# Kernel optimization log

Measured on AMD Instinct MI355X. Metric: run time of the kernel, lower is better.

The kernel has to match this reference:

```python
import jax, jax.numpy as jnp
import numpy as np

N = 6000          # nodes
E = 192000        # edges (avg degree 32)
D = 512           # input_dim
H = 512           # hidden_dim
O = 40            # output_dim (classes)
K = 4096          # codebook_size
LAMB_EDGE = 1.0
LAMB_NODE = 1.0
COMMIT_W = 0.25
EPS = 1e-12


def _graph_conv(x, W, b, src, dst):
    """DGL GraphConv with norm='both' + ReLU activation.
    out = relu( D_in^{-1/2} A D_out^{-1/2} x W + b )"""
    ones = jnp.ones((E,), x.dtype)
    deg_out = jnp.clip(jax.ops.segment_sum(ones, src, num_segments=N), 1.0)
    deg_in = jnp.clip(jax.ops.segment_sum(ones, dst, num_segments=N), 1.0)
    xs = x * jax.lax.rsqrt(deg_out)[:, None]          # scale by src out-degree
    agg = jax.ops.segment_sum(xs[src], dst, num_segments=N)  # gather-scatter
    agg = agg * jax.lax.rsqrt(deg_in)[:, None]        # scale by dst in-degree
    return jax.nn.relu(agg @ W + b)


def _l2norm(x):
    return x * jax.lax.rsqrt(jnp.sum(x * x, axis=-1, keepdims=True) + EPS)


def setup_inputs() -> dict:
    key = jax.random.key(0)
    ks = jax.random.split(key, 13)
    s = lambda d: 1.0 / np.sqrt(d)
    return {
        "feats": jax.random.normal(ks[0], (N, D), jnp.float32),
        "W1": jax.random.normal(ks[1], (D, D), jnp.float32) * s(D),
        "b1": jnp.zeros((D,), jnp.float32),
        "W2": jax.random.normal(ks[2], (D, H), jnp.float32) * s(D),
        "b2": jnp.zeros((H,), jnp.float32),
        "Wd1": jax.random.normal(ks[3], (D, D), jnp.float32) * s(D),
        "bd1": jnp.zeros((D,), jnp.float32),
        "Wd2": jax.random.normal(ks[4], (D, D), jnp.float32) * s(D),
        "bd2": jnp.zeros((D,), jnp.float32),
        "Wl": jax.random.normal(ks[5], (H, O), jnp.float32) * s(H),
        "bl": jnp.zeros((O,), jnp.float32),
        "codebook": jax.random.normal(ks[6], (K, D), jnp.float32),
        "src": jax.random.randint(ks[7], (E,), 0, N, jnp.int32),
        "dst": jax.random.randint(ks[8], (E,), 0, N, jnp.int32),
    }


def reference(feats, W1, b1, W2, b2, Wd1, bd1, Wd2, bd2, Wl, bl, codebook, src, dst):
    # dense adjacency (as the torch module materializes via to_dense())
    adj = jnp.zeros((N, N), feats.dtype).at[dst, src].add(1.0)

    # GraphConv layer 1 (dropout is identity in eval)
    h = _graph_conv(feats, W1, b1, src, dst)           # [N, D]

    # cosine-sim VectorQuantize
    hn = _l2norm(h)
    en = _l2norm(codebook)                             # [K, D]
    dist = hn @ en.T                                   # [N, K] cosine sims
    ind = jnp.argmax(dist, axis=-1)                    # [N]
    q = en[ind]                                        # quantize with normed codebook
    commit_loss = COMMIT_W * jnp.mean((jax.lax.stop_gradient(q) - h) ** 2)
    quantized = h + jax.lax.stop_gradient(q - h)       # straight-through

    quantized_edge = quantized @ Wd1 + bd1             # decoder_1
    quantized_node = quantized @ Wd2 + bd2             # decoder_2

    feature_rec_loss = LAMB_NODE * jnp.mean((h - quantized_node) ** 2)

    adj_q = quantized_edge @ quantized_edge.T          # [N, N]
    adj_q = (adj_q - adj_q.min()) / (adj_q.max() - adj_q.min())
    edge_rec_loss = LAMB_EDGE * jnp.sqrt(jnp.mean((adj - adj_q) ** 2))

    # GraphConv layer 2 + output linear
    h2 = _graph_conv(quantized_edge, W2, b2, src, dst) # [N, H]
    out = h2 @ Wl + bl                                 # [N, O]

    loss = feature_rec_loss + edge_rec_loss + commit_loss
    return out, loss, dist
```

## Files before the change

kernel.cpp:

```cpp
#include <hip/hip_runtime.h>

typedef unsigned int u32;
typedef unsigned long long u64;

#define NN_ 6000
#define EE_ 192000
#define DD_ 512
#define KK_ 4096
#define OO_ 40
#define HSZ (1 << 19)
#define HMASK (HSZ - 1)
#define MT_A 376
#define NB_N 47

typedef __bf16 bf16x8 __attribute__((ext_vector_type(8)));
typedef float f32x4 __attribute__((ext_vector_type(4)));
typedef float f32x2 __attribute__((ext_vector_type(2)));

__device__ __forceinline__ u32 okey(float f) {
    u32 u = __float_as_uint(f);
    return (u & 0x80000000u) ? ~u : (u | 0x80000000u);
}
__device__ __forceinline__ float dkey(u32 u) {
    u32 b = (u & 0x80000000u) ? (u ^ 0x80000000u) : ~u;
    return __uint_as_float(b);
}
__device__ __forceinline__ u64 packKey(float v, int col) {
    return ((u64)okey(v) << 32) | (u32)(~(u32)col);
}
__device__ __forceinline__ unsigned short f2bf_rne(float f) {
    u32 x = __float_as_uint(f);
    u32 r = x + 0x7fffu + ((x >> 16) & 1u);
    return (unsigned short)(r >> 16);
}
__device__ __forceinline__ void gld_lds16(void* l, const void* g) {
    __builtin_amdgcn_global_load_lds(
        (const __attribute__((address_space(1))) unsigned int*)g,
        (__attribute__((address_space(3))) unsigned int*)l, 16, 0, 0);
}
__device__ __forceinline__ void gl8(
    const void* p0, const void* p1, const void* p2, const void* p3,
    const void* p4, const void* p5, const void* p6, const void* p7,
    f32x2& v0, f32x2& v1, f32x2& v2, f32x2& v3,
    f32x2& v4, f32x2& v5, f32x2& v6, f32x2& v7) {
    asm volatile(
        "global_load_dwordx2 %0, %8, off\n\t"
        "global_load_dwordx2 %1, %9, off\n\t"
        "global_load_dwordx2 %2, %10, off\n\t"
        "global_load_dwordx2 %3, %11, off\n\t"
        "global_load_dwordx2 %4, %12, off\n\t"
        "global_load_dwordx2 %5, %13, off\n\t"
        "global_load_dwordx2 %6, %14, off\n\t"
        "global_load_dwordx2 %7, %15, off\n\t"
        "s_waitcnt vmcnt(0)"
        : "=&v"(v0), "=&v"(v1), "=&v"(v2), "=&v"(v3),
          "=&v"(v4), "=&v"(v5), "=&v"(v6), "=&v"(v7)
        : "v"(p0), "v"(p1), "v"(p2), "v"(p3),
          "v"(p4), "v"(p5), "v"(p6), "v"(p7)
        : "memory");
}
__device__ __forceinline__ void split8(const float* vals, uint4& hw, uint4& lw) {
    u32 h[4], l[4];
    #pragma unroll
    for (int j = 0; j < 4; ++j) {
        unsigned short h0 = f2bf_rne(vals[2*j]),   h1 = f2bf_rne(vals[2*j+1]);
        float hf0 = __uint_as_float((u32)h0 << 16), hf1 = __uint_as_float((u32)h1 << 16);
        unsigned short l0 = f2bf_rne(vals[2*j] - hf0), l1 = f2bf_rne(vals[2*j+1] - hf1);
        h[j] = (u32)h0 | ((u32)h1 << 16);
        l[j] = (u32)l0 | ((u32)l1 << 16);
    }
    hw = make_uint4(h[0], h[1], h[2], h[3]);
    lw = make_uint4(l[0], l[1], l[2], l[3]);
}

__global__ void k_deg(const int* __restrict__ src, const int* __restrict__ dst,
                      int* __restrict__ degout, int* __restrict__ degin) {
    int e = blockIdx.x * 256 + threadIdx.x;
    if (e >= EE_) return;
    atomicAdd(&degout[src[e]], 1);
    atomicAdd(&degin[dst[e]], 1);
}

__global__ void k_rsqrtdeg(const int* __restrict__ degout, const int* __restrict__ degin,
                           float* __restrict__ rout, float* __restrict__ rin) {
    int i = blockIdx.x * 256 + threadIdx.x;
    if (i >= NN_) return;
    int doV = degout[i]; if (doV < 1) doV = 1;
    int diV = degin[i];  if (diV < 1) diV = 1;
    rout[i] = rsqrtf((float)doV);
    rin[i]  = rsqrtf((float)diV);
}

__global__ void k_scan(const int* __restrict__ cnt, int* __restrict__ offs, int n) {
    __shared__ int buf[1024];
    __shared__ int carry;
    if (threadIdx.x == 0) { carry = 0; offs[0] = 0; }
    __syncthreads();
    for (int base = 0; base < n; base += 1024) {
        int i = base + threadIdx.x;
        int v = (i < n) ? cnt[i] : 0;
        buf[threadIdx.x] = v;
        __syncthreads();
        for (int off = 1; off < 1024; off <<= 1) {
            int t = (threadIdx.x >= off) ? buf[threadIdx.x - off] : 0;
            __syncthreads();
            buf[threadIdx.x] += t;
            __syncthreads();
        }
        if (i < n) offs[i + 1] = carry + buf[threadIdx.x];
        __syncthreads();
        if (threadIdx.x == 0) carry += buf[1023];
        __syncthreads();
    }
}

__global__ void k_fill(const int* __restrict__ src, const int* __restrict__ dst,
                       const int* __restrict__ offs, int* __restrict__ cursor,
                       int* __restrict__ esrc) {
    int e = blockIdx.x * 256 + threadIdx.x;
    if (e >= EE_) return;
    int d = dst[e];
    int pos = offs[d] + atomicAdd(&cursor[d], 1);
    esrc[pos] = src[e];
}

__device__ __forceinline__ void pack_row_from_lds(
    const float* rowbuf, int node, int t,
    unsigned short* __restrict__ dh, unsigned short* __restrict__ dl) {
    int kb = t >> 2, sub = t & 3;
    int lane = sub * 16 + (node & 15);
    uint4 hw, lw;
    split8(rowbuf + t * 8, hw, lw);
    size_t base = (((size_t)(node >> 4) * 16 + kb) * 64 + lane) * 8;
    *(uint4*)(dh + base) = hw;
    *(uint4*)(dl + base) = lw;
}

__global__ __launch_bounds__(256) void k_aggp(
    const float* __restrict__ X, const int* __restrict__ esrc,
    const int* __restrict__ offs, const float* __restrict__ rout,
    const float* __restrict__ rin,
    unsigned short* __restrict__ dh, unsigned short* __restrict__ dl) {
    __shared__ float rowbuf[512];
    int node = blockIdx.x;
    int beg = offs[node], end = offs[node + 1];
    int t = threadIdx.x;
    float a0 = 0.f, a1 = 0.f, b0 = 0.f, b1 = 0.f;
    float c0 = 0.f, c1 = 0.f, d0 = 0.f, d1 = 0.f;
    int e = beg;
    for (; e + 8 <= end; e += 8) {
        int s0 = esrc[e+0], s1 = esrc[e+1], s2 = esrc[e+2], s3 = esrc[e+3];
        int s4 = esrc[e+4], s5 = esrc[e+5], s6 = esrc[e+6], s7 = esrc[e+7];
        f32x2 v0, v1, v2, v3, v4, v5, v6, v7;
        gl8(X + (size_t)s0 * DD_ + 2 * t, X + (size_t)s1 * DD_ + 2 * t,
            X + (size_t)s2 * DD_ + 2 * t, X + (size_t)s3 * DD_ + 2 * t,
            X + (size_t)s4 * DD_ + 2 * t, X + (size_t)s5 * DD_ + 2 * t,
            X + (size_t)s6 * DD_ + 2 * t, X + (size_t)s7 * DD_ + 2 * t,
            v0, v1, v2, v3, v4, v5, v6, v7);
        float w0 = rout[s0], w1 = rout[s1], w2 = rout[s2], w3 = rout[s3];
        float w4 = rout[s4], w5 = rout[s5], w6 = rout[s6], w7 = rout[s7];
        a0 = fmaf(w0, v0[0], a0); a1 = fmaf(w0, v0[1], a1);
        b0 = fmaf(w1, v1[0], b0); b1 = fmaf(w1, v1[1], b1);
        c0 = fmaf(w2, v2[0], c0); c1 = fmaf(w2, v2[1], c1);
        d0 = fmaf(w3, v3[0], d0); d1 = fmaf(w3, v3[1], d1);
        a0 = fmaf(w4, v4[0], a0); a1 = fmaf(w4, v4[1], a1);
        b0 = fmaf(w5, v5[0], b0); b1 = fmaf(w5, v5[1], b1);
        c0 = fmaf(w6, v6[0], c0); c1 = fmaf(w6, v6[1], c1);
        d0 = fmaf(w7, v7[0], d0); d1 = fmaf(w7, v7[1], d1);
    }
    for (; e < end; ++e) {
        int s = esrc[e];
        float w = rout[s];
        float2 v = ((const float2*)(X + (size_t)s * DD_))[t];
        a0 = fmaf(w, v.x, a0); a1 = fmaf(w, v.y, a1);
    }
    float ri = rin[node];
    rowbuf[2 * t] = (a0 + b0 + c0 + d0) * ri;
    rowbuf[2 * t + 1] = (a1 + b1 + c1 + d1) * ri;
    __syncthreads();
    if (t < 64) pack_row_from_lds(rowbuf, node, t, dh, dl);
}

__global__ __launch_bounds__(256) void k_aggd(
    const float* __restrict__ QE, const int* __restrict__ esrc,
    const int* __restrict__ offs, const float* __restrict__ rout,
    const float* __restrict__ rin,
    unsigned short* __restrict__ dh, unsigned short* __restrict__ dl,
    float* __restrict__ gacc) {
    __shared__ float rowbuf[512];
    __shared__ float wred[4];
    int node = blockIdx.x;
    int beg = offs[node], end = offs[node + 1];
    int t = threadIdx.x;
    float a0 = 0.f, a1 = 0.f, b0 = 0.f, b1 = 0.f;
    float c0 = 0.f, c1 = 0.f, d0 = 0.f, d1 = 0.f;
    float ua0 = 0.f, ua1 = 0.f, ub0 = 0.f, ub1 = 0.f;
    int e = beg;
    for (; e + 8 <= end; e += 8) {
        int s0 = esrc[e+0], s1 = esrc[e+1], s2 = esrc[e+2], s3 = esrc[e+3];
        int s4 = esrc[e+4], s5 = esrc[e+5], s6 = esrc[e+6], s7 = esrc[e+7];
        f32x2 v0, v1, v2, v3, v4, v5, v6, v7;
        gl8(QE + (size_t)s0 * DD_ + 2 * t, QE + (size_t)s1 * DD_ + 2 * t,
            QE + (size_t)s2 * DD_ + 2 * t, QE + (size_t)s3 * DD_ + 2 * t,
            QE + (size_t)s4 * DD_ + 2 * t, QE + (size_t)s5 * DD_ + 2 * t,
            QE + (size_t)s6 * DD_ + 2 * t, QE + (size_t)s7 * DD_ + 2 * t,
            v0, v1, v2, v3, v4, v5, v6, v7);
        float w0 = rout[s0], w1 = rout[s1], w2 = rout[s2], w3 = rout[s3];
        float w4 = rout[s4], w5 = rout[s5], w6 = rout[s6], w7 = rout[s7];
        a0 = fmaf(w0, v0[0], a0); a1 = fmaf(w0, v0[1], a1);
        b0 = fmaf(w1, v1[0], b0); b1 = fmaf(w1, v1[1], b1);
        c0 = fmaf(w2, v2[0], c0); c1 = fmaf(w2, v2[1], c1);
        d0 = fmaf(w3, v3[0], d0); d1 = fmaf(w3, v3[1], d1);
        a0 = fmaf(w4, v4[0], a0); a1 = fmaf(w4, v4[1], a1);
        b0 = fmaf(w5, v5[0], b0); b1 = fmaf(w5, v5[1], b1);
        c0 = fmaf(w6, v6[0], c0); c1 = fmaf(w6, v6[1], c1);
        d0 = fmaf(w7, v7[0], d0); d1 = fmaf(w7, v7[1], d1);
        ua0 += v0[0] + v2[0] + v4[0] + v6[0];
        ua1 += v0[1] + v2[1] + v4[1] + v6[1];
        ub0 += v1[0] + v3[0] + v5[0] + v7[0];
        ub1 += v1[1] + v3[1] + v5[1] + v7[1];
    }
    for (; e < end; ++e) {
        int s = esrc[e];
        float w = rout[s];
        float2 v = ((const float2*)(QE + (size_t)s * DD_))[t];
        a0 = fmaf(w, v.x, a0); a1 = fmaf(w, v.y, a1);
        ua0 += v.x; ua1 += v.y;
    }
    float ri = rin[node];
    rowbuf[2 * t] = (a0 + b0 + c0 + d0) * ri;
    rowbuf[2 * t + 1] = (a1 + b1 + c1 + d1) * ri;
    float2 q = ((const float2*)(QE + (size_t)node * DD_))[t];
    float c = q.x * (ua0 + ub0) + q.y * (ua1 + ub1);
    for (int off = 32; off; off >>= 1) c += __shfl_xor(c, off);
    int lane = t & 63, wv = t >> 6;
    if (lane == 0) wred[wv] = c;
    __syncthreads();
    if (t < 64) pack_row_from_lds(rowbuf, node, t, dh, dl);
    if (t == 0) atomicAdd(&gacc[5], wred[0] + wred[1] + wred[2] + wred[3]);
}

__global__ __launch_bounds__(256) void k_cbscale(const float* __restrict__ cb, float* __restrict__ scale) {
    int row = blockIdx.x;
    float2 v = ((const float2*)(cb + (size_t)row * DD_))[threadIdx.x];
    float s = v.x * v.x + v.y * v.y;
    for (int off = 32; off; off >>= 1) s += __shfl_xor(s, off);
    __shared__ float wsum[4];
    int lane = threadIdx.x & 63, wv = threadIdx.x >> 6;
    if (lane == 0) wsum[wv] = s;
    __syncthreads();
    if (threadIdx.x == 0) scale[row] = 1.0f / sqrtf(wsum[0] + wsum[1] + wsum[2] + wsum[3] + 1e-12f);
}

__global__ __launch_bounds__(256) void k_pack(
    const float* __restrict__ src, const float* __restrict__ rowscale,
    const int* __restrict__ gidx, int nrows,
    unsigned short* __restrict__ dh, unsigned short* __restrict__ dl) {
    int u = threadIdx.x >> 6, lane = threadIdx.x & 63;
    int mt = blockIdx.x, kb = blockIdx.y * 4 + u;
    int gr = mt * 16 + (lane & 15);
    int k = kb * 32 + (lane >> 4) * 8;
    float vals[8] = {0.f,0.f,0.f,0.f,0.f,0.f,0.f,0.f};
    if (gr < nrows) {
        int row = gidx ? gidx[gr] : gr;
        float sc = rowscale ? rowscale[row] : 1.0f;
        const float4* p = (const float4*)(src + (size_t)row * DD_ + k);
        float4 a = p[0], b = p[1];
        vals[0]=a.x*sc; vals[1]=a.y*sc; vals[2]=a.z*sc; vals[3]=a.w*sc;
        vals[4]=b.x*sc; vals[5]=b.y*sc; vals[6]=b.z*sc; vals[7]=b.w*sc;
    }
    uint4 hw, lw;
    split8(vals, hw, lw);
    size_t base = (((size_t)mt * 16 + kb) * 64 + lane) * 8;
    *(uint4*)(dh + base) = hw;
    *(uint4*)(dl + base) = lw;
}

__global__ __launch_bounds__(256) void k_wpack(
    const float* __restrict__ W,
    unsigned short* __restrict__ dh, unsigned short* __restrict__ dl) {
    int u = threadIdx.x >> 6, lane = threadIdx.x & 63;
    int mt = blockIdx.x, kb = blockIdx.y * 4 + u;
    int n = mt * 16 + (lane & 15);
    int k = kb * 32 + (lane >> 4) * 8;
    float vals[8];
    #pragma unroll
    for (int j = 0; j < 8; ++j) vals[j] = W[(size_t)(k + j) * DD_ + n];
    uint4 hw, lw;
    split8(vals, hw, lw);
    size_t base = (((size_t)mt * 16 + kb) * 64 + lane) * 8;
    *(uint4*)(dh + base) = hw;
    *(uint4*)(dl + base) = lw;
}

template<int MODE>
__global__ __launch_bounds__(256) void gemm_mfma(
    const unsigned short* __restrict__ Ah, const unsigned short* __restrict__ Al,
    const unsigned short* __restrict__ Bh, const unsigned short* __restrict__ Bl,
    float* __restrict__ Cout, const float* __restrict__ bias,
    const float* __restrict__ Ref, int relu, int Mrows,
    float* __restrict__ gacc, u32* __restrict__ minKey, u32* __restrict__ maxKey) {
    if (MODE == 1 && blockIdx.x < blockIdx.y) return;
    __shared__ char lds[32768];
    int tid = threadIdx.x;
    int wave = tid >> 6, lane = tid & 63;
    int gmtA = blockIdx.y * 8, gmtB = blockIdx.x * 8;
    const unsigned short* garr; int gmt0;
    if (wave == 0)      { garr = Ah; gmt0 = gmtA; }
    else if (wave == 1) { garr = Al; gmt0 = gmtA; }
    else if (wave == 2) { garr = Bh; gmt0 = gmtB; }
    else                { garr = Bl; gmt0 = gmtB; }
    char* ldst = lds + wave * 8192;
    f32x4 acc[4][4];
    #pragma unroll
    for (int i = 0; i < 4; ++i)
        #pragma unroll
        for (int j = 0; j < 4; ++j) acc[i][j] = (f32x4){0.f, 0.f, 0.f, 0.f};
    int wm = wave >> 1, wn = wave & 1;
    for (int kb = 0; kb < 16; ++kb) {
        #pragma unroll
        for (int t = 0; t < 8; ++t) {
            const char* g = (const char*)garr + (((size_t)(gmt0 + t) * 16 + kb) * 1024) + lane * 16;
            gld_lds16(ldst + t * 1024 + lane * 16, g);
        }
        __syncthreads();
        bf16x8 a_h[4], a_l[4], b_h[4], b_l[4];
        #pragma unroll
        for (int i = 0; i < 4; ++i) {
            int at = wm * 4 + i, bt = wn * 4 + i;
            a_h[i] = *(const bf16x8*)(lds + 0     + at * 1024 + lane * 16);
            a_l[i] = *(const bf16x8*)(lds + 8192  + at * 1024 + lane * 16);
            b_h[i] = *(const bf16x8*)(lds + 16384 + bt * 1024 + lane * 16);
            b_l[i] = *(const bf16x8*)(lds + 24576 + bt * 1024 + lane * 16);
        }
        #pragma unroll
        for (int i = 0; i < 4; ++i)
            #pragma unroll
            for (int j = 0; j < 4; ++j) {
                acc[i][j] = __builtin_amdgcn_mfma_f32_16x16x32_bf16(a_h[i], b_h[j], acc[i][j], 0, 0, 0);
                acc[i][j] = __builtin_amdgcn_mfma_f32_16x16x32_bf16(a_h[i], b_l[j], acc[i][j], 0, 0, 0);
                acc[i][j] = __builtin_amdgcn_mfma_f32_16x16x32_bf16(a_l[i], b_h[j], acc[i][j], 0, 0, 0);
            }
        __syncthreads();
    }
    int m_base = blockIdx.y * 128 + wm * 64;
    int n_base = blockIdx.x * 128 + wn * 64;
    int rq = lane >> 4, cc = lane & 15;
    if (MODE == 0) {
        #pragma unroll
        for (int i = 0; i < 4; ++i) {
            int m = m_base + i * 16 + rq * 4;
            #pragma unroll
            for (int j = 0; j < 4; ++j) {
                int n = n_base + j * 16 + cc;
                #pragma unroll
                for (int r = 0; r < 4; ++r) {
                    if (m + r < NN_) Cout[(size_t)(m + r) * KK_ + n] = acc[i][j][r];
                }
            }
        }
    } else if (MODE == 2) {
        #pragma unroll
        for (int i = 0; i < 4; ++i) {
            int m = m_base + i * 16 + rq * 4;
            #pragma unroll
            for (int j = 0; j < 4; ++j) {
                int n = n_base + j * 16 + cc;
                float bv = bias[n];
                #pragma unroll
                for (int r = 0; r < 4; ++r) {
                    if (m + r < Mrows) {
                        float v = acc[i][j][r] + bv;
                        if (relu) v = fmaxf(v, 0.f);
                        Cout[(size_t)(m + r) * DD_ + n] = v;
                    }
                }
            }
        }
    } else if (MODE == 3) {
        float s = 0.f;
        #pragma unroll
        for (int i = 0; i < 4; ++i) {
            int m = m_base + i * 16 + rq * 4;
            #pragma unroll
            for (int j = 0; j < 4; ++j) {
                int n = n_base + j * 16 + cc;
                float bv = bias[n];
                #pragma unroll
                for (int r = 0; r < 4; ++r) {
                    if (m + r < Mrows) {
                        float d = Ref[(size_t)(m + r) * DD_ + n] - (acc[i][j][r] + bv);
                        s = fmaf(d, d, s);
// ... 145 lines not shown
        int m = m0 + (ty << 2) + i;
        if (m >= M) continue;
        #pragma unroll
        for (int j = 0; j < 4; ++j) {
            int n = n0 + (tx << 2) + j;
            if (n >= Ncols) continue;
            C[(size_t)m * Ncols + n] = cv[i][j] + bias[n];
        }
    }
}

__global__ __launch_bounds__(256) void k_losses(
    const float* __restrict__ h, const float* __restrict__ cb,
    const float* __restrict__ scale, const int* __restrict__ ind,
    float* __restrict__ gacc) {
    float s1 = 0.f;
    for (int idx = blockIdx.x * 256 + threadIdx.x; idx < NN_ * DD_; idx += gridDim.x * 256) {
        int m = idx >> 9, d = idx & 511;
        int r = ind[m];
        float q = cb[(size_t)r * DD_ + d] * scale[r];
        float dq = q - h[idx];
        s1 = fmaf(dq, dq, s1);
    }
    for (int off = 32; off; off >>= 1) s1 += __shfl_xor(s1, off);
    __shared__ float w1[4];
    int lane = threadIdx.x & 63, wv = threadIdx.x >> 6;
    if (lane == 0) w1[wv] = s1;
    __syncthreads();
    if (threadIdx.x == 0) atomicAdd(&gacc[2], w1[0] + w1[1] + w1[2] + w1[3]);
}

__global__ void k_hash(const int* __restrict__ src, const int* __restrict__ dst,
                       int* __restrict__ hkey, int* __restrict__ hcnt) {
    int e = blockIdx.x * 256 + threadIdx.x;
    if (e >= EE_) return;
    int key = dst[e] * NN_ + src[e];
    u32 h = ((u32)key * 2654435761u) & HMASK;
    while (true) {
        int old = atomicCAS(&hkey[h], -1, key);
        if (old == -1 || old == key) { atomicAdd(&hcnt[h], 1); break; }
        h = (h + 1) & HMASK;
    }
}

__global__ __launch_bounds__(256) void k_m2scan(const int* __restrict__ hcnt, float* __restrict__ gacc) {
    float s = 0.f;
    for (int i = blockIdx.x * 256 + threadIdx.x; i < HSZ; i += gridDim.x * 256) {
        float c = (float)hcnt[i];
        s = fmaf(c, c, s);
    }
    for (int off = 32; off; off >>= 1) s += __shfl_xor(s, off);
    __shared__ float w1[4];
    int lane = threadIdx.x & 63, wv = threadIdx.x >> 6;
    if (lane == 0) w1[wv] = s;
    __syncthreads();
    if (threadIdx.x == 0) atomicAdd(&gacc[4], w1[0] + w1[1] + w1[2] + w1[3]);
}

__global__ void k_final(const float* __restrict__ gacc, const u32* __restrict__ minKey,
                        const u32* __restrict__ maxKey, float* __restrict__ lossOut) {
    if (threadIdx.x != 0 || blockIdx.x != 0) return;
    double Rsum = gacc[0], Rsq = gacc[1], commitS = gacc[2], recS = gacc[3];
    double m2 = gacc[4], mr = gacc[5], ms = (double)EE_;
    double mn = (double)dkey(*minKey);
    double mx = (double)dkey(*maxKey);
    double den = mx - mn;
    double NN2 = (double)NN_ * (double)NN_;
    double sum_aq2 = (Rsq - 2.0 * mn * Rsum + NN2 * mn * mn) / (den * den);
    double sum_maq = (mr - mn * ms) / den;
    double total = sum_aq2 + m2 - 2.0 * sum_maq;
    double edge = sqrt(total / NN2);
    double commit = 0.25 * commitS / ((double)NN_ * (double)DD_);
    double rec = recS / ((double)NN_ * (double)DD_);
    *lossOut = (float)(rec + edge + commit);
}

extern "C" void kernel_launch(void* const* d_in, const int* in_sizes, int n_in,
                              void* d_out, int out_size, void* d_ws, size_t ws_size,
                              hipStream_t stream) {
    const float* feats = (const float*)d_in[0];
    const float* W1 = (const float*)d_in[1];
    const float* b1 = (const float*)d_in[2];
    const float* W2 = (const float*)d_in[3];
    const float* b2v = (const float*)d_in[4];
    const float* Wd1 = (const float*)d_in[5];
    const float* bd1 = (const float*)d_in[6];
    const float* Wd2 = (const float*)d_in[7];
    const float* bd2 = (const float*)d_in[8];
    const float* Wl = (const float*)d_in[9];
    const float* bl = (const float*)d_in[10];
    const float* cb = (const float*)d_in[11];
    const int* src = (const int*)d_in[12];
    const int* dst = (const int*)d_in[13];

    float* outF = (float*)d_out;
    float* lossOut = outF + (size_t)NN_ * OO_;
    float* distOut = lossOut + 1;

    char* w = (char*)d_ws;
    size_t off = 0;
    auto alloc = [&](size_t bytes) -> void* {
        void* p = w + off;
        off = (off + bytes + 255) & ~(size_t)255;
        return p;
    };
    float* gacc = (float*)alloc(64);
    u32* maxKey = (u32*)alloc(4);
    int* degin = (int*)alloc((size_t)NN_ * 4);
    int* degout = (int*)alloc((size_t)NN_ * 4);
    int* cursor = (int*)alloc((size_t)NN_ * 4);
    int* hcnt = (int*)alloc((size_t)HSZ * 4);
    size_t z0end = off;
    int* hkey = (int*)alloc((size_t)HSZ * 4);
    u32* minKey = (u32*)alloc(4);
    size_t z1end = off;
    int* offs = (int*)alloc((size_t)(NN_ + 1) * 4);
    int* esrc = (int*)alloc((size_t)EE_ * 4);
    float* rin = (float*)alloc((size_t)NN_ * 4);
    float* rout = (float*)alloc((size_t)NN_ * 4);
    int* ind = (int*)alloc((size_t)NN_ * 4);
    float* scale = (float*)alloc((size_t)KK_ * 4);
    float* rnorm = (float*)alloc((size_t)NN_ * 4);
    float* h = (float*)alloc((size_t)NN_ * DD_ * 4);
    float* QE = (float*)alloc((size_t)NN_ * DD_ * 4);
    const size_t NPACK = (size_t)MT_A * 16 * DD_;
    unsigned short* P1 = (unsigned short*)alloc(NPACK * 2 * 2);
    unsigned short* P2 = (unsigned short*)alloc(NPACK * 2 * 2);
    unsigned short* enp = (unsigned short*)alloc((size_t)KK_ * DD_ * 2 * 2);
    const size_t WPACK = (size_t)32 * 16 * DD_;
    unsigned short* W1p = (unsigned short*)alloc(WPACK * 2 * 2);
    unsigned short* Wd1p = (unsigned short*)alloc(WPACK * 2 * 2);
    unsigned short* Wd2p = (unsigned short*)alloc(WPACK * 2 * 2);
    unsigned short* W2p = (unsigned short*)alloc(WPACK * 2 * 2);

    unsigned short* aggp_h = P1,  *aggp_l = P1 + NPACK;
    unsigned short* qcp_h  = P1,  *qcp_l  = P1 + NPACK;
    unsigned short* ag2p_h = P1,  *ag2p_l = P1 + NPACK;
    unsigned short* hnp_h  = P2,  *hnp_l  = P2 + NPACK;
    unsigned short* QEp_h  = P2,  *QEp_l  = P2 + NPACK;
    unsigned short* enp_h  = enp, *enp_l  = enp + (size_t)KK_ * DD_;

    hipMemsetAsync(w, 0, z0end, stream);
    hipMemsetAsync(w + z0end, 0xFF, z1end - z0end, stream);

    const int TB = 256;
    k_deg<<<(EE_ + TB - 1) / TB, TB, 0, stream>>>(src, dst, degout, degin);
    k_rsqrtdeg<<<(NN_ + TB - 1) / TB, TB, 0, stream>>>(degout, degin, rout, rin);
    k_scan<<<1, 1024, 0, stream>>>(degin, offs, NN_);
    k_fill<<<(EE_ + TB - 1) / TB, TB, 0, stream>>>(src, dst, offs, cursor, esrc);
    k_wpack<<<dim3(32, 4), TB, 0, stream>>>(W1, W1p, W1p + WPACK);
    k_wpack<<<dim3(32, 4), TB, 0, stream>>>(Wd1, Wd1p, Wd1p + WPACK);
    k_wpack<<<dim3(32, 4), TB, 0, stream>>>(Wd2, Wd2p, Wd2p + WPACK);
    k_wpack<<<dim3(32, 4), TB, 0, stream>>>(W2, W2p, W2p + WPACK);
    k_aggp<<<NN_, TB, 0, stream>>>(feats, esrc, offs, rout, rin, aggp_h, aggp_l);
    gemm_mfma<2><<<dim3(4, NB_N), TB, 0, stream>>>(aggp_h, aggp_l, W1p, W1p + WPACK,
                                                   h, b1, nullptr, 1, NN_, nullptr, nullptr, nullptr);
    k_cbscale<<<NN_, TB, 0, stream>>>(h, rnorm);
    k_cbscale<<<KK_, TB, 0, stream>>>(cb, scale);
    k_pack<<<dim3(MT_A, 4), TB, 0, stream>>>(h, rnorm, nullptr, NN_, hnp_h, hnp_l);
    k_pack<<<dim3(KK_ / 16, 4), TB, 0, stream>>>(cb, scale, nullptr, KK_, enp_h, enp_l);
    gemm_mfma<0><<<dim3(KK_ / 128, NB_N), TB, 0, stream>>>(hnp_h, hnp_l, enp_h, enp_l,
                                                           distOut, nullptr, nullptr, 0, NN_,
                                                           nullptr, nullptr, nullptr);
    k_rescore<<<NN_, TB, 0, stream>>>(distOut, h, rnorm, cb, scale, ind);
    k_pack<<<dim3(MT_A, 4), TB, 0, stream>>>(cb, scale, ind, NN_, qcp_h, qcp_l);
    gemm_mfma<2><<<dim3(4, NB_N), TB, 0, stream>>>(qcp_h, qcp_l, Wd1p, Wd1p + WPACK,
                                                   QE, bd1, nullptr, 0, NN_, nullptr, nullptr, nullptr);
    gemm_mfma<3><<<dim3(4, NB_N), TB, 0, stream>>>(qcp_h, qcp_l, Wd2p, Wd2p + WPACK,
                                                   nullptr, bd2, h, 0, NN_, gacc, nullptr, nullptr);
    k_losses<<<2048, TB, 0, stream>>>(h, cb, scale, ind, gacc);
    k_pack<<<dim3(MT_A, 4), TB, 0, stream>>>(QE, nullptr, nullptr, NN_, QEp_h, QEp_l);
    gemm_mfma<1><<<dim3(NB_N, NB_N), TB, 0, stream>>>(QEp_h, QEp_l, QEp_h, QEp_l,
                                                      nullptr, nullptr, nullptr, 0, NN_,
                                                      gacc, minKey, maxKey);
    k_hash<<<(EE_ + TB - 1) / TB, TB, 0, stream>>>(src, dst, hkey, hcnt);
    k_m2scan<<<512, TB, 0, stream>>>(hcnt, gacc);
    k_aggd<<<NN_, TB, 0, stream>>>(QE, esrc, offs, rout, rin, ag2p_h, ag2p_l, gacc);
    gemm_mfma<2><<<dim3(4, NB_N), TB, 0, stream>>>(ag2p_h, ag2p_l, W2p, W2p + WPACK,
                                                   h, b2v, nullptr, 1, NN_, nullptr, nullptr, nullptr);
    gemm_nn<<<dim3(1, 94), TB, 0, stream>>>(h, Wl, bl, outF, NN_, OO_, DD_);
    k_final<<<1, 64, 0, stream>>>(gacc, minKey, maxKey, lossOut);
}
```

Before: 758.3 us.

## Double-buffer neighbor-row gathers into LDS via async global-to-LDS loads

Rewrites the two aggregation kernels so each block first stages neighbor indices and weights in shared memory. Neighbor feature rows are then copied in chunks of 8 with global_load_lds into a double-buffered LDS tile, so the load of the next chunk overlaps the FMA work on the current one. This replaces the previous register gather with a blocking vmcnt(0) wait after every 8 rows. It adds 32KB of LDS per block plus extra barriers, which can lower occupancy for these gather-bound kernels.

```diff
diff --git a/kernel.cpp b/kernel.cpp
--- a/kernel.cpp
+++ b/kernel.cpp
@@ -38,27 +38,133 @@
         (const __attribute__((address_space(1))) unsigned int*)g,
         (__attribute__((address_space(3))) unsigned int*)l, 16, 0, 0);
 }
-__device__ __forceinline__ void gl8(
-    const void* p0, const void* p1, const void* p2, const void* p3,
-    const void* p4, const void* p5, const void* p6, const void* p7,
-    f32x2& v0, f32x2& v1, f32x2& v2, f32x2& v3,
-    f32x2& v4, f32x2& v5, f32x2& v6, f32x2& v7) {
-    asm volatile(
-        "global_load_dwordx2 %0, %8, off\n\t"
-        "global_load_dwordx2 %1, %9, off\n\t"
-        "global_load_dwordx2 %2, %10, off\n\t"
-        "global_load_dwordx2 %3, %11, off\n\t"
-        "global_load_dwordx2 %4, %12, off\n\t"
-        "global_load_dwordx2 %5, %13, off\n\t"
-        "global_load_dwordx2 %6, %14, off\n\t"
-        "global_load_dwordx2 %7, %15, off\n\t"
-        "s_waitcnt vmcnt(0)"
-        : "=&v"(v0), "=&v"(v1), "=&v"(v2), "=&v"(v3),
-          "=&v"(v4), "=&v"(v5), "=&v"(v6), "=&v"(v7)
-        : "v"(p0), "v"(p1), "v"(p2), "v"(p3),
-          "v"(p4), "v"(p5), "v"(p6), "v"(p7)
-        : "memory");
-}
+
+#define WVMC4 do { asm volatile("s_waitcnt vmcnt(4)" ::: "memory"); __builtin_amdgcn_sched_barrier(0); } while (0)
+#define WVMC0 do { asm volatile("s_waitcnt vmcnt(0)" ::: "memory"); __builtin_amdgcn_sched_barrier(0); } while (0)
+#define LGKM0 do { asm volatile("s_waitcnt lgkmcnt(0)" ::: "memory"); __builtin_amdgcn_sched_barrier(0); } while (0)
+#define BARR  do { __builtin_amdgcn_sched_barrier(0); __builtin_amdgcn_s_barrier(); __builtin_amdgcn_sched_barrier(0); } while (0)
+
+__device__ __forceinline__ void stage_chunk(
+    const float* __restrict__ X, const int* sidx, int base,
+    float* dst, int w, int lane) {
+    #pragma unroll
+    for (int rr = 0; rr < 2; ++rr) {
+        int r = 2 * w + rr;
+        int s = sidx[base + r];
+        const float* g = X + (size_t)s * DD_ + lane * 4;
+        float* d = dst + r * DD_;
+        gld_lds16(d, g);
+        gld_lds16(d + 256, g + 256);
+    }
+}
+
+template<int UNW>
+__device__ __forceinline__ void consume_chunk(
+    const float* xb, const float* swt, int base, int t,
+    float& o0, float& o1, float& u0, float& u1) {
+    #pragma unroll
+    for (int r = 0; r < 8; ++r) {
+        float w = swt[base + r];
+        float2 v = *(const float2*)(xb + r * DD_ + 2 * t);
+        o0 = fmaf(w, v.x, o0);
+        o1 = fmaf(w, v.y, o1);
+        if (UNW) { u0 += v.x; u1 += v.y; }
+    }
+}
+
+template<int UNW>
+__device__ __forceinline__ void agg_lds(
+    const float* __restrict__ X, const int* sidx, const float* swt,
+    float* xbuf , int scnt, int t,
+    float& o0, float& o1, float& u0, float& u1) {
+    int w = t >> 6, lane = t & 63;
+    int nch = scnt >> 3;
+    float* b0 = xbuf;
+    float* b1 = xbuf + 8 * DD_;
+    if (nch > 0) {
+        stage_chunk(X, sidx, 0, b0, w, lane);
+        if (nch > 1) {
+            stage_chunk(X, sidx, 8, b1, w, lane);
+            WVMC4;
+        } else {
+            WVMC0;
+        }
+        BARR;
+        int c = 0;
+        for (; c + 2 < nch; ++c) {
+            float* cur = (c & 1) ? b1 : b0;
+            consume_chunk<UNW>(cur, swt, c * 8, t, o0, o1, u0, u1);
+            LGKM0; BARR;
+            stage_chunk(X, sidx, (c + 2) * 8, cur, w, lane);
+            WVMC4; BARR;
+        }
+        consume_chunk<UNW>((c & 1) ? b1 : b0, swt, c * 8, t, o0, o1, u0, u1);
+        ++c;
+        if (c < nch) {
+            WVMC0; BARR;
+            consume_chunk<UNW>((c & 1) ? b1 : b0, swt, c * 8, t, o0, o1, u0, u1);
+        }
+    }
+    for (int i = nch * 8; i < scnt; ++i) {
+        float wgt = swt[i];
+        float2 v = ((const float2*)(X + (size_t)sidx[i] * DD_))[t];
+        o0 = fmaf(wgt, v.x, o0);
+        o1 = fmaf(wgt, v.y, o1);
+        if (UNW) { u0 += v.x; u1 += v.y; }
+    }
+}
+
+__global__ void k_deg(const int* __restrict__ src, const int* __restrict__ dst,
+                      int* __restrict__ degout, int* __restrict__ degin) {
+    int e = blockIdx.x * 256 + threadIdx.x;
+    if (e >= EE_) return;
+    atomicAdd(&degout[src[e]], 1);
+    atomicAdd(&degin[dst[e]], 1);
+}
+
+__global__ void k_rsqrtdeg(const int* __restrict__ degout, const int* __restrict__ degin,
+                           float* __restrict__ rout, float* __restrict__ rin) {
+    int i = blockIdx.x * 256 + threadIdx.x;
+    if (i >= NN_) return;
+    int doV = degout[i]; if (doV < 1) doV = 1;
+    int diV = degin[i];  if (diV < 1) diV = 1;
+    rout[i] = rsqrtf((float)doV);
+    rin[i]  = rsqrtf((float)diV);
+}
+
+__global__ void k_scan(const int* __restrict__ cnt, int* __restrict__ offs, int n) {
+    __shared__ int buf[1024];
+    __shared__ int carry;
+    if (threadIdx.x == 0) { carry = 0; offs[0] = 0; }
+    __syncthreads();
+    for (int base = 0; base < n; base += 1024) {
+        int i = base + threadIdx.x;
+        int v = (i < n) ? cnt[i] : 0;
+        buf[threadIdx.x] = v;
+        __syncthreads();
+        for (int off = 1; off < 1024; off <<= 1) {
+            int t = (threadIdx.x >= off) ? buf[threadIdx.x - off] : 0;
+            __syncthreads();
+            buf[threadIdx.x] += t;
+            __syncthreads();
+        }
+        if (i < n) offs[i + 1] = carry + buf[threadIdx.x];
+        __syncthreads();
+        if (threadIdx.x == 0) carry += buf[1023];
+        __syncthreads();
+    }
+}
+
+__global__ void k_fill(const int* __restrict__ src, const int* __restrict__ dst,
+                       const int* __restrict__ offs, int* __restrict__ cursor,
+                       int* __restrict__ esrc) {
+    int e = blockIdx.x * 256 + threadIdx.x;
+    if (e >= EE_) return;
+    int d = dst[e];
+    int pos = offs[d] + atomicAdd(&cursor[d], 1);
+    esrc[pos] = src[e];
+}
+
 __device__ __forceinline__ void split8(const float* vals, uint4& hw, uint4& lw) {
     u32 h[4], l[4];
     #pragma unroll
@@ -71,57 +177,6 @@
     }
     hw = make_uint4(h[0], h[1], h[2], h[3]);
     lw = make_uint4(l[0], l[1], l[2], l[3]);
-}
-
-__global__ void k_deg(const int* __restrict__ src, const int* __restrict__ dst,
-                      int* __restrict__ degout, int* __restrict__ degin) {
-    int e = blockIdx.x * 256 + threadIdx.x;
-    if (e >= EE_) return;
-    atomicAdd(&degout[src[e]], 1);
-    atomicAdd(&degin[dst[e]], 1);
-}
-
-__global__ void k_rsqrtdeg(const int* __restrict__ degout, const int* __restrict__ degin,
-                           float* __restrict__ rout, float* __restrict__ rin) {
-    int i = blockIdx.x * 256 + threadIdx.x;
-    if (i >= NN_) return;
-    int doV = degout[i]; if (doV < 1) doV = 1;
-    int diV = degin[i];  if (diV < 1) diV = 1;
-    rout[i] = rsqrtf((float)doV);
-    rin[i]  = rsqrtf((float)diV);
-}
-
-__global__ void k_scan(const int* __restrict__ cnt, int* __restrict__ offs, int n) {
-    __shared__ int buf[1024];
-    __shared__ int carry;
-    if (threadIdx.x == 0) { carry = 0; offs[0] = 0; }
-    __syncthreads();
-    for (int base = 0; base < n; base += 1024) {
-        int i = base + threadIdx.x;
-        int v = (i < n) ? cnt[i] : 0;
-        buf[threadIdx.x] = v;
-        __syncthreads();
-        for (int off = 1; off < 1024; off <<= 1) {
-            int t = (threadIdx.x >= off) ? buf[threadIdx.x - off] : 0;
-            __syncthreads();
-            buf[threadIdx.x] += t;
-            __syncthreads();
-        }
-        if (i < n) offs[i + 1] = carry + buf[threadIdx.x];
-        __syncthreads();
-        if (threadIdx.x == 0) carry += buf[1023];
-        __syncthreads();
-    }
-}
-
-__global__ void k_fill(const int* __restrict__ src, const int* __restrict__ dst,
-                       const int* __restrict__ offs, int* __restrict__ cursor,
-                       int* __restrict__ esrc) {
-    int e = blockIdx.x * 256 + threadIdx.x;
-    if (e >= EE_) return;
-    int d = dst[e];
-    int pos = offs[d] + atomicAdd(&cursor[d], 1);
-    esrc[pos] = src[e];
 }
 
 __device__ __forceinline__ void pack_row_from_lds(
@@ -141,42 +196,28 @@
     const int* __restrict__ offs, const float* __restrict__ rout,
     const float* __restrict__ rin,
     unsigned short* __restrict__ dh, unsigned short* __restrict__ dl) {
+    __shared__ float xbuf[2][8][DD_];
     __shared__ float rowbuf[512];
+    __shared__ int sidx[256];
+    __shared__ float swt[256];
     int node = blockIdx.x;
     int beg = offs[node], end = offs[node + 1];
+    int deg = end - beg;
     int t = threadIdx.x;
-    float a0 = 0.f, a1 = 0.f, b0 = 0.f, b1 = 0.f;
-    float c0 = 0.f, c1 = 0.f, d0 = 0.f, d1 = 0.f;
-    int e = beg;
-    for (; e + 8 <= end; e += 8) {
-        int s0 = esrc[e+0], s1 = esrc[e+1], s2 = esrc[e+2], s3 = esrc[e+3];
-        int s4 = esrc[e+4], s5 = esrc[e+5], s6 = esrc[e+6], s7 = esrc[e+7];
-        f32x2 v0, v1, v2, v3, v4, v5, v6, v7;
-        gl8(X + (size_t)s0 * DD_ + 2 * t, X + (size_t)s1 * DD_ + 2 * t,
-            X + (size_t)s2 * DD_ + 2 * t, X + (size_t)s3 * DD_ + 2 * t,
-            X + (size_t)s4 * DD_ + 2 * t, X + (size_t)s5 * DD_ + 2 * t,
-            X + (size_t)s6 * DD_ + 2 * t, X + (size_t)s7 * DD_ + 2 * t,
-            v0, v1, v2, v3, v4, v5, v6, v7);
-        float w0 = rout[s0], w1 = rout[s1], w2 = rout[s2], w3 = rout[s3];
-        float w4 = rout[s4], w5 = rout[s5], w6 = rout[s6], w7 = rout[s7];
-        a0 = fmaf(w0, v0[0], a0); a1 = fmaf(w0, v0[1], a1);
-        b0 = fmaf(w1, v1[0], b0); b1 = fmaf(w1, v1[1], b1);
-        c0 = fmaf(w2, v2[0], c0); c1 = fmaf(w2, v2[1], c1);
-        d0 = fmaf(w3, v3[0], d0); d1 = fmaf(w3, v3[1], d1);
-        a0 = fmaf(w4, v4[0], a0); a1 = fmaf(w4, v4[1], a1);
-        b0 = fmaf(w5, v5[0], b0); b1 = fmaf(w5, v5[1], b1);
-        c0 = fmaf(w6, v6[0], c0); c1 = fmaf(w6, v6[1], c1);
-        d0 = fmaf(w7, v7[0], d0); d1 = fmaf(w7, v7[1], d1);
-    }
-    for (; e < end; ++e) {
+    int scnt = deg < 256 ? deg : 256;
+    if (t < scnt) { int s = esrc[beg + t]; sidx[t] = s; swt[t] = rout[s]; }
+    __syncthreads();
+    float o0 = 0.f, o1 = 0.f, u0 = 0.f, u1 = 0.f;
+    agg_lds<0>(X, sidx, swt, &xbuf[0][0][0], scnt, t, o0, o1, u0, u1);
+    for (int e = beg + 256; e < end; ++e) {
         int s = esrc[e];
         float w = rout[s];
         float2 v = ((const float2*)(X + (size_t)s * DD_))[t];
-        a0 = fmaf(w, v.x, a0); a1 = fmaf(w, v.y, a1);
+        o0 = fmaf(w, v.x, o0); o1 = fmaf(w, v.y, o1);
     }
     float ri = rin[node];
-    rowbuf[2 * t] = (a0 + b0 + c0 + d0) * ri;
-    rowbuf[2 * t + 1] = (a1 + b1 + c1 + d1) * ri;
+    rowbuf[2 * t] = o0 * ri;
+    rowbuf[2 * t + 1] = o1 * ri;
     __syncthreads();
     if (t < 64) pack_row_from_lds(rowbuf, node, t, dh, dl);
 }
@@ -187,51 +228,32 @@
     const float* __restrict__ rin,
     unsigned short* __restrict__ dh, unsigned short* __restrict__ dl,
     float* __restrict__ gacc) {
+    __shared__ float xbuf[2][8][DD_];
     __shared__ float rowbuf[512];
     __shared__ float wred[4];
+    __shared__ int sidx[256];
+    __shared__ float swt[256];
     int node = blockIdx.x;
     int beg = offs[node], end = offs[node + 1];
+    int deg = end - beg;
     int t = threadIdx.x;
-    float a0 = 0.f, a1 = 0.f, b0 = 0.f, b1 = 0.f;
-    float c0 = 0.f, c1 = 0.f, d0 = 0.f, d1 = 0.f;
-    float ua0 = 0.f, ua1 = 0.f, ub0 = 0.f, ub1 = 0.f;
-    int e = beg;
-    for (; e + 8 <= end; e += 8) {
-        int s0 = esrc[e+0], s1 = esrc[e+1], s2 = esrc[e+2], s3 = esrc[e+3];
-        int s4 = esrc[e+4], s5 = esrc[e+5], s6 = esrc[e+6], s7 = esrc[e+7];
-        f32x2 v0, v1, v2, v3, v4, v5, v6, v7;
-        gl8(QE + (size_t)s0 * DD_ + 2 * t, QE + (size_t)s1 * DD_ + 2 * t,
-            QE + (size_t)s2 * DD_ + 2 * t, QE + (size_t)s3 * DD_ + 2 * t,
-            QE + (size_t)s4 * DD_ + 2 * t, QE + (size_t)s5 * DD_ + 2 * t,
-            QE + (size_t)s6 * DD_ + 2 * t, QE + (size_t)s7 * DD_ + 2 * t,
-            v0, v1, v2, v3, v4, v5, v6, v7);
-        float w0 = rout[s0], w1 = rout[s1], w2 = rout[s2], w3 = rout[s3];
-        float w4 = rout[s4], w5 = rout[s5], w6 = rout[s6], w7 = rout[s7];
-        a0 = fmaf(w0, v0[0], a0); a1 = fmaf(w0, v0[1], a1);
-        b0 = fmaf(w1, v1[0], b0); b1 = fmaf(w1, v1[1], b1);
-        c0 = fmaf(w2, v2[0], c0); c1 = fmaf(w2, v2[1], c1);
-        d0 = fmaf(w3, v3[0], d0); d1 = fmaf(w3, v3[1], d1);
-        a0 = fmaf(w4, v4[0], a0); a1 = fmaf(w4, v4[1], a1);
-        b0 = fmaf(w5, v5[0], b0); b1 = fmaf(w5, v5[1], b1);
-        c0 = fmaf(w6, v6[0], c0); c1 = fmaf(w6, v6[1], c1);
-        d0 = fmaf(w7, v7[0], d0); d1 = fmaf(w7, v7[1], d1);
-        ua0 += v0[0] + v2[0] + v4[0] + v6[0];
-        ua1 += v0[1] + v2[1] + v4[1] + v6[1];
-        ub0 += v1[0] + v3[0] + v5[0] + v7[0];
-        ub1 += v1[1] + v3[1] + v5[1] + v7[1];
-    }
-    for (; e < end; ++e) {
+    int scnt = deg < 256 ? deg : 256;
+    if (t < scnt) { int s = esrc[beg + t]; sidx[t] = s; swt[t] = rout[s]; }
+    __syncthreads();
+    float o0 = 0.f, o1 = 0.f, u0 = 0.f, u1 = 0.f;
+    agg_lds<1>(QE, sidx, swt, &xbuf[0][0][0], scnt, t, o0, o1, u0, u1);
+    for (int e = beg + 256; e < end; ++e) {
         int s = esrc[e];
         float w = rout[s];
         float2 v = ((const float2*)(QE + (size_t)s * DD_))[t];
-        a0 = fmaf(w, v.x, a0); a1 = fmaf(w, v.y, a1);
-        ua0 += v.x; ua1 += v.y;
+        o0 = fmaf(w, v.x, o0); o1 = fmaf(w, v.y, o1);
+        u0 += v.x; u1 += v.y;
     }
     float ri = rin[node];
-    rowbuf[2 * t] = (a0 + b0 + c0 + d0) * ri;
-    rowbuf[2 * t + 1] = (a1 + b1 + c1 + d1) * ri;
+    rowbuf[2 * t] = o0 * ri;
+    rowbuf[2 * t + 1] = o1 * ri;
     float2 q = ((const float2*)(QE + (size_t)node * DD_))[t];
-    float c = q.x * (ua0 + ub0) + q.y * (ua1 + ub1);
+    float c = q.x * u0 + q.y * u1;
     for (int off = 32; off; off >>= 1) c += __shfl_xor(c, off);
     int lane = t & 63, wv = t >> 6;
     if (lane == 0) wred[wv] = c;
```

New measurement: 750.4 us. No clear change (-1.0%).

## Split neighbor aggregation across four column slices with LDS-staged edge indices

Applied to the files above, without the earlier changes.

Replaces the two per-node aggregation kernels with one templated kernel. Each node's 512 columns are now split into four 128-column slices, one block per slice, and each block's four waves work on different edges. Source indices and their out-degree weights are staged in shared memory first. The per-wave partial sums are then reduced in LDS before packing to split bf16. This is meant to expose more parallelism and shorten the serial per-edge dependency chain. The cost is four times as many blocks, repeated index loads per slice, and the loss of the hand-batched eight-way inline-asm loads.

```diff
diff --git a/kernel.cpp b/kernel.cpp
--- a/kernel.cpp
+++ b/kernel.cpp
@@ -15,7 +15,6 @@
 
 typedef __bf16 bf16x8 __attribute__((ext_vector_type(8)));
 typedef float f32x4 __attribute__((ext_vector_type(4)));
-typedef float f32x2 __attribute__((ext_vector_type(2)));
 
 __device__ __forceinline__ u32 okey(float f) {
     u32 u = __float_as_uint(f);
@@ -38,27 +37,58 @@
         (const __attribute__((address_space(1))) unsigned int*)g,
         (__attribute__((address_space(3))) unsigned int*)l, 16, 0, 0);
 }
-__device__ __forceinline__ void gl8(
-    const void* p0, const void* p1, const void* p2, const void* p3,
-    const void* p4, const void* p5, const void* p6, const void* p7,
-    f32x2& v0, f32x2& v1, f32x2& v2, f32x2& v3,
-    f32x2& v4, f32x2& v5, f32x2& v6, f32x2& v7) {
-    asm volatile(
-        "global_load_dwordx2 %0, %8, off\n\t"
-        "global_load_dwordx2 %1, %9, off\n\t"
-        "global_load_dwordx2 %2, %10, off\n\t"
-        "global_load_dwordx2 %3, %11, off\n\t"
-        "global_load_dwordx2 %4, %12, off\n\t"
-        "global_load_dwordx2 %5, %13, off\n\t"
-        "global_load_dwordx2 %6, %14, off\n\t"
-        "global_load_dwordx2 %7, %15, off\n\t"
-        "s_waitcnt vmcnt(0)"
-        : "=&v"(v0), "=&v"(v1), "=&v"(v2), "=&v"(v3),
-          "=&v"(v4), "=&v"(v5), "=&v"(v6), "=&v"(v7)
-        : "v"(p0), "v"(p1), "v"(p2), "v"(p3),
-          "v"(p4), "v"(p5), "v"(p6), "v"(p7)
-        : "memory");
-}
+
+__global__ void k_deg(const int* __restrict__ src, const int* __restrict__ dst,
+                      int* __restrict__ degout, int* __restrict__ degin) {
+    int e = blockIdx.x * 256 + threadIdx.x;
+    if (e >= EE_) return;
+    atomicAdd(&degout[src[e]], 1);
+    atomicAdd(&degin[dst[e]], 1);
+}
+
+__global__ void k_rsqrtdeg(const int* __restrict__ degout, const int* __restrict__ degin,
+                           float* __restrict__ rout, float* __restrict__ rin) {
+    int i = blockIdx.x * 256 + threadIdx.x;
+    if (i >= NN_) return;
+    int doV = degout[i]; if (doV < 1) doV = 1;
+    int diV = degin[i];  if (diV < 1) diV = 1;
+    rout[i] = rsqrtf((float)doV);
+    rin[i]  = rsqrtf((float)diV);
+}
+
+__global__ void k_scan(const int* __restrict__ cnt, int* __restrict__ offs, int n) {
+    __shared__ int buf[1024];
+    __shared__ int carry;
+    if (threadIdx.x == 0) { carry = 0; offs[0] = 0; }
+    __syncthreads();
+    for (int base = 0; base < n; base += 1024) {
+        int i = base + threadIdx.x;
+        int v = (i < n) ? cnt[i] : 0;
+        buf[threadIdx.x] = v;
+        __syncthreads();
+        for (int off = 1; off < 1024; off <<= 1) {
+            int t = (threadIdx.x >= off) ? buf[threadIdx.x - off] : 0;
+            __syncthreads();
+            buf[threadIdx.x] += t;
+            __syncthreads();
+        }
+        if (i < n) offs[i + 1] = carry + buf[threadIdx.x];
+        __syncthreads();
+        if (threadIdx.x == 0) carry += buf[1023];
+        __syncthreads();
+    }
+}
+
+__global__ void k_fill(const int* __restrict__ src, const int* __restrict__ dst,
+                       const int* __restrict__ offs, int* __restrict__ cursor,
+                       int* __restrict__ esrc) {
+    int e = blockIdx.x * 256 + threadIdx.x;
+    if (e >= EE_) return;
+    int d = dst[e];
+    int pos = offs[d] + atomicAdd(&cursor[d], 1);
+    esrc[pos] = src[e];
+}
+
 __device__ __forceinline__ void split8(const float* vals, uint4& hw, uint4& lw) {
     u32 h[4], l[4];
     #pragma unroll
@@ -73,171 +103,75 @@
     lw = make_uint4(l[0], l[1], l[2], l[3]);
 }
 
-__global__ void k_deg(const int* __restrict__ src, const int* __restrict__ dst,
-                      int* __restrict__ degout, int* __restrict__ degin) {
-    int e = blockIdx.x * 256 + threadIdx.x;
-    if (e >= EE_) return;
-    atomicAdd(&degout[src[e]], 1);
-    atomicAdd(&degin[dst[e]], 1);
-}
-
-__global__ void k_rsqrtdeg(const int* __restrict__ degout, const int* __restrict__ degin,
-                           float* __restrict__ rout, float* __restrict__ rin) {
-    int i = blockIdx.x * 256 + threadIdx.x;
-    if (i >= NN_) return;
-    int doV = degout[i]; if (doV < 1) doV = 1;
-    int diV = degin[i];  if (diV < 1) diV = 1;
-    rout[i] = rsqrtf((float)doV);
-    rin[i]  = rsqrtf((float)diV);
-}
-
-__global__ void k_scan(const int* __restrict__ cnt, int* __restrict__ offs, int n) {
-    __shared__ int buf[1024];
-    __shared__ int carry;
-    if (threadIdx.x == 0) { carry = 0; offs[0] = 0; }
-    __syncthreads();
-    for (int base = 0; base < n; base += 1024) {
-        int i = base + threadIdx.x;
-        int v = (i < n) ? cnt[i] : 0;
-        buf[threadIdx.x] = v;
-        __syncthreads();
-        for (int off = 1; off < 1024; off <<= 1) {
-            int t = (threadIdx.x >= off) ? buf[threadIdx.x - off] : 0;
-            __syncthreads();
-            buf[threadIdx.x] += t;
-            __syncthreads();
-        }
-        if (i < n) offs[i + 1] = carry + buf[threadIdx.x];
-        __syncthreads();
-        if (threadIdx.x == 0) carry += buf[1023];
-        __syncthreads();
-    }
-}
-
-__global__ void k_fill(const int* __restrict__ src, const int* __restrict__ dst,
-                       const int* __restrict__ offs, int* __restrict__ cursor,
-                       int* __restrict__ esrc) {
-    int e = blockIdx.x * 256 + threadIdx.x;
-    if (e >= EE_) return;
-    int d = dst[e];
-    int pos = offs[d] + atomicAdd(&cursor[d], 1);
-    esrc[pos] = src[e];
-}
-
-__device__ __forceinline__ void pack_row_from_lds(
-    const float* rowbuf, int node, int t,
-    unsigned short* __restrict__ dh, unsigned short* __restrict__ dl) {
-    int kb = t >> 2, sub = t & 3;
-    int lane = sub * 16 + (node & 15);
-    uint4 hw, lw;
-    split8(rowbuf + t * 8, hw, lw);
-    size_t base = (((size_t)(node >> 4) * 16 + kb) * 64 + lane) * 8;
-    *(uint4*)(dh + base) = hw;
-    *(uint4*)(dl + base) = lw;
-}
-
-__global__ __launch_bounds__(256) void k_aggp(
+template<int UNW>
+__global__ __launch_bounds__(256) void k_aggs(
     const float* __restrict__ X, const int* __restrict__ esrc,
-    const int* __restrict__ offs, const float* __restrict__ rout,
-    const float* __restrict__ rin,
-    unsigned short* __restrict__ dh, unsigned short* __restrict__ dl) {
-    __shared__ float rowbuf[512];
-    int node = blockIdx.x;
-    int beg = offs[node], end = offs[node + 1];
-    int t = threadIdx.x;
-    float a0 = 0.f, a1 = 0.f, b0 = 0.f, b1 = 0.f;
-    float c0 = 0.f, c1 = 0.f, d0 = 0.f, d1 = 0.f;
-    int e = beg;
-    for (; e + 8 <= end; e += 8) {
-        int s0 = esrc[e+0], s1 = esrc[e+1], s2 = esrc[e+2], s3 = esrc[e+3];
-        int s4 = esrc[e+4], s5 = esrc[e+5], s6 = esrc[e+6], s7 = esrc[e+7];
-        f32x2 v0, v1, v2, v3, v4, v5, v6, v7;
-        gl8(X + (size_t)s0 * DD_ + 2 * t, X + (size_t)s1 * DD_ + 2 * t,
-            X + (size_t)s2 * DD_ + 2 * t, X + (size_t)s3 * DD_ + 2 * t,
-            X + (size_t)s4 * DD_ + 2 * t, X + (size_t)s5 * DD_ + 2 * t,
-            X + (size_t)s6 * DD_ + 2 * t, X + (size_t)s7 * DD_ + 2 * t,
-            v0, v1, v2, v3, v4, v5, v6, v7);
-        float w0 = rout[s0], w1 = rout[s1], w2 = rout[s2], w3 = rout[s3];
-        float w4 = rout[s4], w5 = rout[s5], w6 = rout[s6], w7 = rout[s7];
-        a0 = fmaf(w0, v0[0], a0); a1 = fmaf(w0, v0[1], a1);
-        b0 = fmaf(w1, v1[0], b0); b1 = fmaf(w1, v1[1], b1);
-        c0 = fmaf(w2, v2[0], c0); c1 = fmaf(w2, v2[1], c1);
-        d0 = fmaf(w3, v3[0], d0); d1 = fmaf(w3, v3[1], d1);
-        a0 = fmaf(w4, v4[0], a0); a1 = fmaf(w4, v4[1], a1);
-        b0 = fmaf(w5, v5[0], b0); b1 = fmaf(w5, v5[1], b1);
-        c0 = fmaf(w6, v6[0], c0); c1 = fmaf(w6, v6[1], c1);
-        d0 = fmaf(w7, v7[0], d0); d1 = fmaf(w7, v7[1], d1);
-    }
-    for (; e < end; ++e) {
-        int s = esrc[e];
-        float w = rout[s];
-        float2 v = ((const float2*)(X + (size_t)s * DD_))[t];
-        a0 = fmaf(w, v.x, a0); a1 = fmaf(w, v.y, a1);
-    }
-    float ri = rin[node];
-    rowbuf[2 * t] = (a0 + b0 + c0 + d0) * ri;
-    rowbuf[2 * t + 1] = (a1 + b1 + c1 + d1) * ri;
-    __syncthreads();
-    if (t < 64) pack_row_from_lds(rowbuf, node, t, dh, dl);
-}
-
-__global__ __launch_bounds__(256) void k_aggd(
-    const float* __restrict__ QE, const int* __restrict__ esrc,
     const int* __restrict__ offs, const float* __restrict__ rout,
     const float* __restrict__ rin,
     unsigned short* __restrict__ dh, unsigned short* __restrict__ dl,
     float* __restrict__ gacc) {
-    __shared__ float rowbuf[512];
-    __shared__ float wred[4];
-    int node = blockIdx.x;
+    __shared__ int sidx[256];
+    __shared__ float swt[256];
+    __shared__ float redw[4][128];
+    __shared__ float redu[4][128];
+    int b = blockIdx.x;
+    int x = b & 7;
+    int slice = x >> 1;
+    int node = ((b >> 3) << 1) | (x & 1);
     int beg = offs[node], end = offs[node + 1];
+    int deg = end - beg;
     int t = threadIdx.x;
-    float a0 = 0.f, a1 = 0.f, b0 = 0.f, b1 = 0.f;
-    float c0 = 0.f, c1 = 0.f, d0 = 0.f, d1 = 0.f;
-    float ua0 = 0.f, ua1 = 0.f, ub0 = 0.f, ub1 = 0.f;
-    int e = beg;
-    for (; e + 8 <= end; e += 8) {
-        int s0 = esrc[e+0], s1 = esrc[e+1], s2 = esrc[e+2], s3 = esrc[e+3];
-        int s4 = esrc[e+4], s5 = esrc[e+5], s6 = esrc[e+6], s7 = esrc[e+7];
-        f32x2 v0, v1, v2, v3, v4, v5, v6, v7;
-        gl8(QE + (size_t)s0 * DD_ + 2 * t, QE + (size_t)s1 * DD_ + 2 * t,
-            QE + (size_t)s2 * DD_ + 2 * t, QE + (size_t)s3 * DD_ + 2 * t,
-            QE + (size_t)s4 * DD_ + 2 * t, QE + (size_t)s5 * DD_ + 2 * t,
-            QE + (size_t)s6 * DD_ + 2 * t, QE + (size_t)s7 * DD_ + 2 * t,
-            v0, v1, v2, v3, v4, v5, v6, v7);
-        float w0 = rout[s0], w1 = rout[s1], w2 = rout[s2], w3 = rout[s3];
-        float w4 = rout[s4], w5 = rout[s5], w6 = rout[s6], w7 = rout[s7];
-        a0 = fmaf(w0, v0[0], a0); a1 = fmaf(w0, v0[1], a1);
-        b0 = fmaf(w1, v1[0], b0); b1 = fmaf(w1, v1[1], b1);
-        c0 = fmaf(w2, v2[0], c0); c1 = fmaf(w2, v2[1], c1);
-        d0 = fmaf(w3, v3[0], d0); d1 = fmaf(w3, v3[1], d1);
-        a0 = fmaf(w4, v4[0], a0); a1 = fmaf(w4, v4[1], a1);
-        b0 = fmaf(w5, v5[0], b0); b1 = fmaf(w5, v5[1], b1);
-        c0 = fmaf(w6, v6[0], c0); c1 = fmaf(w6, v6[1], c1);
-        d0 = fmaf(w7, v7[0], d0); d1 = fmaf(w7, v7[1], d1);
-        ua0 += v0[0] + v2[0] + v4[0] + v6[0];
-        ua1 += v0[1] + v2[1] + v4[1] + v6[1];
-        ub0 += v1[0] + v3[0] + v5[0] + v7[0];
-        ub1 += v1[1] + v3[1] + v5[1] + v7[1];
-    }
-    for (; e < end; ++e) {
+    int scnt = deg < 256 ? deg : 256;
+    if (t < scnt) { int s = esrc[beg + t]; sidx[t] = s; swt[t] = rout[s]; }
+    __syncthreads();
+    int cp = t & 63;
+    int ro = t >> 6;
+    int col = slice * 128 + cp * 2;
+    float a0 = 0.f, a1 = 0.f, u0 = 0.f, u1 = 0.f;
+    for (int i = ro; i < scnt; i += 4) {
+        int s = sidx[i];
+        float w = swt[i];
+        float2 v = *(const float2*)(X + (size_t)s * DD_ + col);
+        a0 = fmaf(w, v.x, a0); a1 = fmaf(w, v.y, a1);
+        if (UNW) { u0 += v.x; u1 += v.y; }
+    }
+    for (int e = beg + 256 + ro; e < end; e += 4) {
         int s = esrc[e];
         float w = rout[s];
-        float2 v = ((const float2*)(QE + (size_t)s * DD_))[t];
+        float2 v = *(const float2*)(X + (size_t)s * DD_ + col);
         a0 = fmaf(w, v.x, a0); a1 = fmaf(w, v.y, a1);
-        ua0 += v.x; ua1 += v.y;
-    }
-    float ri = rin[node];
-    rowbuf[2 * t] = (a0 + b0 + c0 + d0) * ri;
-    rowbuf[2 * t + 1] = (a1 + b1 + c1 + d1) * ri;
-    float2 q = ((const float2*)(QE + (size_t)node * DD_))[t];
-    float c = q.x * (ua0 + ub0) + q.y * (ua1 + ub1);
-    for (int off = 32; off; off >>= 1) c += __shfl_xor(c, off);
-    int lane = t & 63, wv = t >> 6;
-    if (lane == 0) wred[wv] = c;
-    __syncthreads();
-    if (t < 64) pack_row_from_lds(rowbuf, node, t, dh, dl);
-    if (t == 0) atomicAdd(&gacc[5], wred[0] + wred[1] + wred[2] + wred[3]);
+        if (UNW) { u0 += v.x; u1 += v.y; }
+    }
+    redw[ro][cp * 2] = a0; redw[ro][cp * 2 + 1] = a1;
+    if (UNW) { redu[ro][cp * 2] = u0; redu[ro][cp * 2 + 1] = u1; }
+    __syncthreads();
+    if (t < 128) {
+        float wsum = redw[0][t] + redw[1][t] + redw[2][t] + redw[3][t];
+        redw[0][t] = wsum * rin[node];
+        if (UNW) {
+            float usum = redu[0][t] + redu[1][t] + redu[2][t] + redu[3][t];
+            float q = X[(size_t)node * DD_ + slice * 128 + t];
+            redu[0][t] = q * usum;
+        }
+    }
+    __syncthreads();
+    if (t < 16) {
+        int kb = slice * 4 + (t >> 2);
+        int sub = t & 3;
+        int lane = sub * 16 + (node & 15);
+        uint4 hw, lw;
+        split8(&redw[0][(t >> 2) * 32 + sub * 8], hw, lw);
+        size_t base = (((size_t)(node >> 4) * 16 + kb) * 64 + lane) * 8;
+        *(uint4*)(dh + base) = hw;
+        *(uint4*)(dl + base) = lw;
+    }
+    if (UNW) {
+        if (t < 64) {
+            float c = redu[0][t] + redu[0][t + 64];
+            for (int off = 32; off; off >>= 1) c += __shfl_xor(c, off);
+            if (t == 0) atomicAdd(&gacc[5], c);
+        }
+    }
 }
 
 __global__ __launch_bounds__(256) void k_cbscale(const float* __restrict__ cb, float* __restrict__ scale) {
@@ -689,7 +623,7 @@
     k_wpack<<<dim3(32, 4), TB, 0, stream>>>(Wd1, Wd1p, Wd1p + WPACK);
     k_wpack<<<dim3(32, 4), TB, 0, stream>>>(Wd2, Wd2p, Wd2p + WPACK);
     k_wpack<<<dim3(32, 4), TB, 0, stream>>>(W2, W2p, W2p + WPACK);
-    k_aggp<<<NN_, TB, 0, stream>>>(feats, esrc, offs, rout, rin, aggp_h, aggp_l);
+    k_aggs<0><<<4 * NN_, TB, 0, stream>>>(feats, esrc, offs, rout, rin, aggp_h, aggp_l, nullptr);
     gemm_mfma<2><<<dim3(4, NB_N), TB, 0, stream>>>(aggp_h, aggp_l, W1p, W1p + WPACK,
                                                    h, b1, nullptr, 1, NN_, nullptr, nullptr, nullptr);
     k_cbscale<<<NN_, TB, 0, stream>>>(h, rnorm);
@@ -712,7 +646,7 @@
                                                       gacc, minKey, maxKey);
     k_hash<<<(EE_ + TB - 1) / TB, TB, 0, stream>>>(src, dst, hkey, hcnt);
     k_m2scan<<<512, TB, 0, stream>>>(hcnt, gacc);
-    k_aggd<<<NN_, TB, 0, stream>>>(QE, esrc, offs, rout, rin, ag2p_h, ag2p_l, gacc);
+    k_aggs<1><<<4 * NN_, TB, 0, stream>>>(QE, esrc, offs, rout, rin, ag2p_h, ag2p_l, gacc);
     gemm_mfma<2><<<dim3(4, NB_N), TB, 0, stream>>>(ag2p_h, ag2p_l, W2p, W2p + WPACK,
                                                    h, b2v, nullptr, 1, NN_, nullptr, nullptr, nullptr);
     gemm_nn<<<dim3(1, 94), TB, 0, stream>>>(h, Wl, bl, outF, NN_, OO_, DD_);
```

Result: slower. 963.1 us (+27.0%).
